# Kernel optimization log

Hardware: AMD Instinct MI355X
Metric: run time of the kernel (lower is better)

The kernel has to match this reference:

```python
import jax, jax.numpy as jnp
import numpy as np

EXPERT_CAPACITY = 1024  # per-batch per-expert capacity (token_priority <= capacity)


def setup_inputs() -> dict:
    key = jax.random.key(0)
    ks = jax.random.split(key, 5)
    B, S, D, FF, E = 2, 4096, 1024, 4096, 8
    return {
        "hidden_states": jax.random.normal(ks[0], (B, S, D), dtype=jnp.float32),
        "gate_w": jax.random.normal(ks[1], (D, E), dtype=jnp.float32) * (1.0 / np.sqrt(D)),
        "w1": jax.random.normal(ks[2], (E, D, FF), dtype=jnp.float32) * (1.0 / np.sqrt(D)),
        "w2": jax.random.normal(ks[3], (E, FF, D), dtype=jnp.float32) * (1.0 / np.sqrt(FF)),
        "w3": jax.random.normal(ks[4], (E, D, FF), dtype=jnp.float32) * (1.0 / np.sqrt(D)),
    }


def reference(hidden_states, gate_w, w1, w2, w3):
    B, S, D = hidden_states.shape
    E = gate_w.shape[1]
    C = EXPERT_CAPACITY

    # ---- route (jitter_noise = 0) ----
    router_logits = jnp.einsum("bsd,de->bse", hidden_states, gate_w)  # [B,S,E]
    router_probs = jax.nn.softmax(router_logits, axis=-1)
    sel = jnp.argmax(router_probs, axis=-1)  # [B,S] top-1 expert
    onehot = jax.nn.one_hot(sel, E, dtype=jnp.int32)  # [B,S,E]
    priority = jnp.cumsum(onehot, axis=1)  # cumsum over sequence (dim=-2)
    # position of token in its chosen expert's buffer (0-based)
    pos = jnp.take_along_axis(priority, sel[..., None], axis=-1)[..., 0] - 1  # [B,S]
    keep = pos < C  # token_priority <= expert_capacity
    max_prob = jnp.max(router_probs, axis=-1, keepdims=True)  # [B,S,1]

    # ---- dispatch: scatter kept tokens into [B,E,C,D]; dropped tokens have pos>=C -> mode='drop'
    b_idx = jnp.broadcast_to(jnp.arange(B)[:, None], (B, S))
    buf = jnp.zeros((B, E, C, D), dtype=hidden_states.dtype)
    buf = buf.at[b_idx, sel, pos].set(hidden_states, mode="drop")

    # ---- per-expert gated MLP (grouped GEMM): act(x@w1) * (x@w3) @ w2 ----
    g = jax.nn.silu(jnp.einsum("becd,edf->becf", buf, w1))
    u = jnp.einsum("becd,edf->becf", buf, w3)
    expert_out = jnp.einsum("becf,efd->becd", g * u, w2)  # [B,E,C,D]

    # ---- combine: kept tokens get expert output, dropped tokens keep hidden_states ----
    pos_g = jnp.minimum(pos, C - 1)  # safe gather index for dropped tokens
    gathered = expert_out[b_idx, sel, pos_g]  # [B,S,D]
    next_states = jnp.where(keep[..., None], gathered, hidden_states)
    out = max_prob * next_states  # dropout is identity (p=0)
    return out, router_logits
```

## Files before the change

kernel.cpp:

```cpp
#include <hip/hip_runtime.h>
#include <hip/hip_bf16.h>
#include <stdint.h>

#define B_  2
#define S_  4096
#define D_  1024
#define FF_ 4096
#define E_  8
#define C_  1024

typedef unsigned short u16;
typedef unsigned int   u32;
typedef float f32x4  __attribute__((ext_vector_type(4)));
typedef short bf16x8 __attribute__((ext_vector_type(8)));
typedef u16   u16x8  __attribute__((ext_vector_type(8)));

static __device__ __forceinline__ u16 f2bf(float f) {
    union { float f; u32 u; } v; v.f = f;
    u32 u = v.u;
    u32 r = (u + 0x7FFFu + ((u >> 16) & 1u)) >> 16;
    return (u16)r;
}

static __device__ __forceinline__ void gload_lds16(const u16* g, u16* l) {
    __builtin_amdgcn_global_load_lds(
        (const __attribute__((address_space(1))) u32*)g,
        (__attribute__((address_space(3))) u32*)l, 16, 0, 0);
}

#define BAR()    asm volatile("s_barrier" ::: "memory")
#define WAITV(n) asm volatile("s_waitcnt vmcnt(" #n ")" ::: "memory")

__global__ __launch_bounds__(256) void transpose_cvt(const float* __restrict__ src,
                                                     u16* __restrict__ dst, int K, int N) {
    __shared__ u16 t[64 * 64];
    size_t mat = (size_t)blockIdx.z * K * N;
    int n0 = blockIdx.x * 64, k0 = blockIdx.y * 64;
    int l = threadIdx.x & 63, w = threadIdx.x >> 6;
#pragma unroll
    for (int p = 0; p < 2; ++p) {
        int k = p * 32 + w * 8 + ((l >> 4) << 1);
        int n = (l & 15) * 4;
        float4 v0 = *(const float4*)&src[mat + (size_t)(k0 + k) * N + n0 + n];
        float4 v1 = *(const float4*)&src[mat + (size_t)(k0 + k + 1) * N + n0 + n];
        float a0[4] = {v0.x, v0.y, v0.z, v0.w};
        float a1[4] = {v1.x, v1.y, v1.z, v1.w};
#pragma unroll
        for (int j = 0; j < 4; ++j) {
            int nn = n + j;
            u32 pk = (u32)f2bf(a0[j]) | ((u32)f2bf(a1[j]) << 16);
            int slot = (k >> 3) ^ ((nn & 7) ^ ((nn >> 3) & 7));
            *(u32*)((char*)t + nn * 128 + slot * 16 + (k & 7) * 2) = pk;
        }
    }
    __syncthreads();
#pragma unroll
    for (int p = 0; p < 2; ++p) {
        int n = p * 32 + (threadIdx.x >> 3);
        int k8 = threadIdx.x & 7;
        int slot = k8 ^ ((n & 7) ^ ((n >> 3) & 7));
        u16x8 v = *(u16x8*)((char*)t + n * 128 + slot * 16);
        *(u16x8*)&dst[mat + (size_t)(n0 + n) * K + k0 + k8 * 8] = v;
    }
}

__global__ __launch_bounds__(256) void router_kernel(const float* __restrict__ hidden,
                                                     const float* __restrict__ gate_w,
                                                     float* __restrict__ logits_out,
                                                     int* __restrict__ sel,
                                                     float* __restrict__ maxp,
                                                     u16* __restrict__ xbf) {
    __shared__ float gw[D_ * E_];
    for (int i = threadIdx.x; i < D_ * E_ / 4; i += 256)
        ((float4*)gw)[i] = ((const float4*)gate_w)[i];
    __syncthreads();

    int wave = threadIdx.x >> 6, lane = threadIdx.x & 63;
    int tok = blockIdx.x * 4 + wave;
    const float* hrow = hidden + (size_t)tok * D_;
    u16* xrow = xbf + (size_t)tok * D_;

    double acc[8] = {0, 0, 0, 0, 0, 0, 0, 0};
#pragma unroll 4
    for (int i = 0; i < D_ / 64; i++) {
        int d = i * 64 + lane;
        float h = hrow[d];
        xrow[d] = f2bf(h);
        const float4* g4 = (const float4*)(gw + d * 8);
        float4 g0 = g4[0], g1 = g4[1];
        acc[0] += (double)h * g0.x; acc[1] += (double)h * g0.y;
        acc[2] += (double)h * g0.z; acc[3] += (double)h * g0.w;
        acc[4] += (double)h * g1.x; acc[5] += (double)h * g1.y;
        acc[6] += (double)h * g1.z; acc[7] += (double)h * g1.w;
    }
#pragma unroll
    for (int off = 32; off > 0; off >>= 1)
#pragma unroll
        for (int e = 0; e < 8; e++)
            acc[e] += __shfl_xor(acc[e], off);

    float l[8];
#pragma unroll
    for (int e = 0; e < 8; e++) l[e] = (float)acc[e];
    if (lane < 8) logits_out[(size_t)tok * 8 + lane] = l[lane];

    int am = 0; float mx = l[0];
#pragma unroll
    for (int e = 1; e < 8; e++) if (l[e] > mx) { mx = l[e]; am = e; }
    float sum = 0.f;
#pragma unroll
    for (int e = 0; e < 8; e++) sum += expf(l[e] - mx);
    if (lane == 0) { sel[tok] = am; maxp[tok] = 1.0f / sum; }
}

__global__ void scan_kernel(const int* __restrict__ sel, int* __restrict__ pos,
                            int* __restrict__ slot_token, int* __restrict__ counts) {
    int wave = threadIdx.x >> 6, lane = threadIdx.x & 63;
    int b = wave;
    int carry[8] = {0, 0, 0, 0, 0, 0, 0, 0};
    unsigned long long below = (lane == 0) ? 0ull : ((~0ull) >> (64 - lane));
    for (int s0 = 0; s0 < S_; s0 += 64) {
        int s = s0 + lane;
        int e = sel[b * S_ + s];
        int p = 0;
#pragma unroll
        for (int ex = 0; ex < 8; ex++) {
            unsigned long long m = __ballot(e == ex);
            if (e == ex) p = carry[ex] + (int)__popcll(m & below);
            carry[ex] += (int)__popcll(m);
        }
        pos[b * S_ + s] = p;
        if (p < C_) slot_token[(b * E_ + e) * C_ + p] = s;
    }
    if (lane < 8) {
        int c = carry[lane];
        counts[b * E_ + lane] = c < C_ ? c : C_;
    }
}

__global__ __launch_bounds__(512, 2) void gemm1_kernel(const u16* __restrict__ x,
                                                       const u16* __restrict__ w1t,
                                                       const u16* __restrict__ w3t,
                                                       const int* __restrict__ slot_token,
                                                       const int* __restrict__ counts,
                                                       u16* __restrict__ hbuf) {
    extern __shared__ u16 lds[];
    int phys = blockIdx.x + 32 * (blockIdx.y + 4 * blockIdx.z);
    int virt = (phys & 7) * 256 + (phys >> 3);
    int bx = virt & 31, by = (virt >> 5) & 3, bz = virt >> 7;

    int z = bz;
    int cnt = counts[z];
    int c0 = by * 256;
    if (c0 >= cnt) return;
    int n0 = bx * 128;
    int b = z >> 3, e = z & 7;

    int tid = threadIdx.x, w = tid >> 6, l = tid & 63;
    int wm = w >> 2, wn = w & 3;

    int arow0 = tid >> 2, arow1 = arow0 + 128;
    int lk = ((tid & 3) ^ ((tid >> 3) & 3)) * 8;
    int as0 = c0 + arow0, as1 = c0 + arow1;
    int tok0 = slot_token[z * C_ + (as0 < cnt ? as0 : 0)];
    int tok1 = slot_token[z * C_ + (as1 < cnt ? as1 : 0)];
    const u16* pA0 = x + ((size_t)(b * S_ + tok0)) * D_ + lk;
    const u16* pA1 = x + ((size_t)(b * S_ + tok1)) * D_ + lk;
    const u16* pB1 = w1t + ((size_t)e * FF_ + n0 + arow0) * D_ + lk;
    const u16* pB3 = w3t + ((size_t)e * FF_ + n0 + arow0) * D_ + lk;
    u32 wsl = (u32)w * 512;

    u32 ck  = (u32)(((l >> 4) ^ ((l >> 1) & 3)) * 8);
    u32 aoff  = (u32)(wm * 128 + (l & 15)) * 32 + ck;
    u32 b1off = 8192  + (u32)(wn * 32 + (l & 15)) * 32 + ck;
    u32 b3off = 12288 + (u32)(wn * 32 + (l & 15)) * 32 + ck;

    auto STAGE = [&](int t) {
        u16* Ls = lds + ((t & 3) << 14);
        int ko = t << 5;
        gload_lds16(pA0 + ko, Ls + wsl);
        gload_lds16(pA1 + ko, Ls + 4096 + wsl);
        gload_lds16(pB1 + ko, Ls + 8192 + wsl);
        gload_lds16(pB3 + ko, Ls + 12288 + wsl);
    };

    f32x4 acc1[8][2] = {};
    f32x4 acc3[8][2] = {};

    constexpr int NK = D_ / 32;
    STAGE(0); STAGE(1); STAGE(2);
    for (int t = 0; t < NK; ++t) {
        if (t + 2 < NK)      { WAITV(8); }
        else if (t + 1 < NK) { WAITV(4); }
        else                 { WAITV(0); }
        BAR();
        if (t + 3 < NK) STAGE(t + 3);
        const u16* Ls = lds + ((t & 3) << 14);
        bf16x8 af[8], b1f[2], b3f[2];
#pragma unroll
        for (int f = 0; f < 8; f++) af[f] = *(const bf16x8*)(Ls + aoff + f * 512);
#pragma unroll
        for (int n = 0; n < 2; n++) {
            b1f[n] = *(const bf16x8*)(Ls + b1off + n * 512);
            b3f[n] = *(const bf16x8*)(Ls + b3off + n * 512);
        }
        __builtin_amdgcn_s_setprio(1);
#pragma unroll
        for (int f = 0; f < 8; f++)
#pragma unroll
            for (int n = 0; n < 2; n++) {
                acc1[f][n] = __builtin_amdgcn_mfma_f32_16x16x32_bf16(af[f], b1f[n], acc1[f][n], 0, 0, 0);
                acc3[f][n] = __builtin_amdgcn_mfma_f32_16x16x32_bf16(af[f], b3f[n], acc3[f][n], 0, 0, 0);
            }
        __builtin_amdgcn_s_setprio(0);
    }

#pragma unroll
    for (int f = 0; f < 8; f++) {
        int row = wm * 128 + f * 16 + ((l >> 4) << 2);
#pragma unroll
        for (int r = 0; r < 4; r++) {
            int slot = c0 + row + r;
            if (slot < cnt) {
                size_t base = ((size_t)z * C_ + slot) * FF_ + n0 + wn * 32 + (l & 15);
#pragma unroll
                for (int n = 0; n < 2; n++) {
                    float g = acc1[f][n][r], uu = acc3[f][n][r];
                    float h = (g / (1.f + __expf(-g))) * uu;
                    hbuf[base + n * 16] = f2bf(h);
                }
            }
        }
    }
}

__global__ __launch_bounds__(512, 2) void gemm2_kernel(const u16* __restrict__ hbuf,
                                                       const u16* __restrict__ w2t,
                                                       const int* __restrict__ slot_token,
                                                       const int* __restrict__ counts,
                                                       const float* __restrict__ maxp,
                                                       float* __restrict__ out) {
    extern __shared__ u16 lds[];
    int phys = blockIdx.x + 4 * (blockIdx.y + 4 * blockIdx.z);
    int virt = (phys & 7) * 32 + (phys >> 3);
    int bx = virt & 3, by = (virt >> 2) & 3, bz = virt >> 4;

    int z = bz;
    int cnt = counts[z];
    int c0 = by * 256;
    if (c0 >= cnt) return;
    int n0 = bx * 256;
    int b = z >> 3, e = z & 7;

    int tid = threadIdx.x, w = tid >> 6, l = tid & 63;
    int wm = w >> 2, wn = w & 3;

    int arow0 = tid >> 2;
    int lk = ((tid & 3) ^ ((tid >> 3) & 3)) * 8;
    const u16* pA0 = hbuf + ((size_t)z * C_ + c0 + arow0) * FF_ + lk;
    const u16* pA1 = pA0 + (size_t)128 * FF_;
    const u16* pB0 = w2t + ((size_t)e * D_ + n0 + arow0) * FF_ + lk;
    const u16* pB1 = pB0 + (size_t)128 * FF_;
    u32 wsl = (u32)w * 512;

    u32 ck  = (u32)(((l >> 4) ^ ((l >> 1) & 3)) * 8);
    u32 aoff = (u32)(wm * 128 + (l & 15)) * 32 + ck;
    u32 boff = 8192 + (u32)(wn * 64 + (l & 15)) * 32 + ck;

    auto STAGE = [&](int t) {
        u16* Ls = lds + ((t & 3) << 14);
        int ko = t << 5;
        gload_lds16(pA0 + ko, Ls + wsl);
        gload_lds16(pA1 + ko, Ls + 4096 + wsl);
        gload_lds16(pB0 + ko, Ls + 8192 + wsl);
        gload_lds16(pB1 + ko, Ls + 12288 + wsl);
    };

    f32x4 acc[8][4] = {};

    constexpr int NK = FF_ / 32;
    STAGE(0); STAGE(1); STAGE(2);
    for (int t = 0; t < NK; ++t) {
        if (t + 2 < NK)      { WAITV(8); }
        else if (t + 1 < NK) { WAITV(4); }
        else                 { WAITV(0); }
        BAR();
        if (t + 3 < NK) STAGE(t + 3);
        const u16* Ls = lds + ((t & 3) << 14);
        bf16x8 af[8], bfv[4];
#pragma unroll
        for (int f = 0; f < 8; f++) af[f] = *(const bf16x8*)(Ls + aoff + f * 512);
#pragma unroll
        for (int n = 0; n < 4; n++) bfv[n] = *(const bf16x8*)(Ls + boff + n * 512);
        __builtin_amdgcn_s_setprio(1);
#pragma unroll
        for (int f = 0; f < 8; f++)
#pragma unroll
            for (int n = 0; n < 4; n++)
                acc[f][n] = __builtin_amdgcn_mfma_f32_16x16x32_bf16(af[f], bfv[n], acc[f][n], 0, 0, 0);
        __builtin_amdgcn_s_setprio(0);
    }

#pragma unroll
    for (int f = 0; f < 8; f++) {
        int row = wm * 128 + f * 16 + ((l >> 4) << 2);
#pragma unroll
        for (int r = 0; r < 4; r++) {
            int slot = c0 + row + r;
            if (slot < cnt) {
                int s = slot_token[z * C_ + slot];
                float sc = maxp[b * S_ + s];
                float* orow = out + ((size_t)b * S_ + s) * D_ + n0 + wn * 64 + (l & 15);
#pragma unroll
                for (int n = 0; n < 4; n++)
                    orow[n * 16] = sc * acc[f][n][r];
            }
        }
    }
}

__global__ __launch_bounds__(256) void combine_dropped(const float* __restrict__ hidden,
                                                       const int* __restrict__ pos,
                                                       const float* __restrict__ maxp,
                                                       float* __restrict__ out) {
    int t = blockIdx.x;
    if (pos[t] < C_) return;
    float sc = maxp[t];
    const float* src = hidden + (size_t)t * D_;
    float* dst = out + (size_t)t * D_;
    for (int d = threadIdx.x; d < D_; d += 256) dst[d] = sc * src[d];
}

extern "C" void kernel_launch(void* const* d_in, const int* in_sizes, int n_in,
                              void* d_out, int out_size, void* d_ws, size_t ws_size,
                              hipStream_t stream) {
    const float* hidden = (const float*)d_in[0];
    const float* gate_w = (const float*)d_in[1];
    const float* w1     = (const float*)d_in[2];
    const float* w2     = (const float*)d_in[3];
    const float* w3     = (const float*)d_in[4];

    float* out        = (float*)d_out;
    float* logits_out = out + (size_t)B_ * S_ * D_;

    char* ws = (char*)d_ws;
    u16* hidden_bf = (u16*)ws;            ws += (size_t)B_ * S_ * D_ * 2;
    u16* w1t       = (u16*)ws;            ws += (size_t)E_ * D_ * FF_ * 2;
    u16* w3t       = (u16*)ws;            ws += (size_t)E_ * D_ * FF_ * 2;
    u16* w2t       = (u16*)ws;            ws += (size_t)E_ * D_ * FF_ * 2;
    u16* hbuf      = (u16*)ws;            ws += (size_t)B_ * E_ * C_ * FF_ * 2;
    int*   sel        = (int*)ws;         ws += (size_t)B_ * S_ * 4;
    int*   pos        = (int*)ws;         ws += (size_t)B_ * S_ * 4;
    float* maxp       = (float*)ws;       ws += (size_t)B_ * S_ * 4;
    int*   slot_token = (int*)ws;         ws += (size_t)B_ * E_ * C_ * 4;
    int*   counts     = (int*)ws;         ws += (size_t)B_ * E_ * 4;

    (void)hipFuncSetAttribute((const void*)gemm1_kernel,
                              hipFuncAttributeMaxDynamicSharedMemorySize, 131072);
    (void)hipFuncSetAttribute((const void*)gemm2_kernel,
                              hipFuncAttributeMaxDynamicSharedMemorySize, 131072);

    router_kernel<<<B_ * S_ / 4, 256, 0, stream>>>(hidden, gate_w, logits_out, sel, maxp, hidden_bf);
    scan_kernel<<<1, 128, 0, stream>>>(sel, pos, slot_token, counts);

    transpose_cvt<<<dim3(FF_ / 64, D_ / 64, E_), 256, 0, stream>>>(w1, w1t, D_, FF_);
    transpose_cvt<<<dim3(FF_ / 64, D_ / 64, E_), 256, 0, stream>>>(w3, w3t, D_, FF_);
    transpose_cvt<<<dim3(D_ / 64, FF_ / 64, E_), 256, 0, stream>>>(w2, w2t, FF_, D_);

    gemm1_kernel<<<dim3(32, 4, 16), 512, 131072, stream>>>(hidden_bf, w1t, w3t, slot_token, counts, hbuf);
    gemm2_kernel<<<dim3(4, 4, 16), 512, 131072, stream>>>(hbuf, w2t, slot_token, counts, maxp, out);
    combine_dropped<<<B_ * S_, 256, 0, stream>>>(hidden, pos, maxp, out);
}
```

Before: 501.2 us.

## Split GEMM k-step into two phases interleaving stage loads with MFMA halves

Each k-iteration of both expert GEMMs is split into two halves. The first half loads half the A fragments and all B fragments, issues the A-tile prefetch for stage t+3, waits on LDS and runs half the MFMAs. A second barrier follows, then the remaining A fragments are read, the B-tile prefetch is issued and the rest of the MFMAs run. The aim is to interleave global-to-LDS traffic with matrix math and spread out LDS reads, at the cost of an extra barrier and explicit lgkmcnt waits per iteration.

```diff
diff --git a/kernel.cpp b/kernel.cpp
--- a/kernel.cpp
+++ b/kernel.cpp
@@ -30,6 +30,8 @@
 
 #define BAR()    asm volatile("s_barrier" ::: "memory")
 #define WAITV(n) asm volatile("s_waitcnt vmcnt(" #n ")" ::: "memory")
+#define WAITL0() do { asm volatile("s_waitcnt lgkmcnt(0)" ::: "memory"); \
+                      __builtin_amdgcn_sched_barrier(0); } while (0)
 
 __global__ __launch_bounds__(256) void transpose_cvt(const float* __restrict__ src,
                                                      u16* __restrict__ dst, int K, int N) {
@@ -175,11 +177,15 @@
     u32 b1off = 8192  + (u32)(wn * 32 + (l & 15)) * 32 + ck;
     u32 b3off = 12288 + (u32)(wn * 32 + (l & 15)) * 32 + ck;
 
-    auto STAGE = [&](int t) {
+    auto STAGE_A = [&](int t) {
         u16* Ls = lds + ((t & 3) << 14);
         int ko = t << 5;
         gload_lds16(pA0 + ko, Ls + wsl);
         gload_lds16(pA1 + ko, Ls + 4096 + wsl);
+    };
+    auto STAGE_B = [&](int t) {
+        u16* Ls = lds + ((t & 3) << 14);
+        int ko = t << 5;
         gload_lds16(pB1 + ko, Ls + 8192 + wsl);
         gload_lds16(pB3 + ko, Ls + 12288 + wsl);
     };
@@ -188,25 +194,40 @@
     f32x4 acc3[8][2] = {};
 
     constexpr int NK = D_ / 32;
-    STAGE(0); STAGE(1); STAGE(2);
+    STAGE_A(0); STAGE_B(0); STAGE_A(1); STAGE_B(1); STAGE_A(2); STAGE_B(2);
     for (int t = 0; t < NK; ++t) {
         if (t + 2 < NK)      { WAITV(8); }
         else if (t + 1 < NK) { WAITV(4); }
         else                 { WAITV(0); }
         BAR();
-        if (t + 3 < NK) STAGE(t + 3);
         const u16* Ls = lds + ((t & 3) << 14);
         bf16x8 af[8], b1f[2], b3f[2];
 #pragma unroll
-        for (int f = 0; f < 8; f++) af[f] = *(const bf16x8*)(Ls + aoff + f * 512);
+        for (int f = 0; f < 4; f++) af[f] = *(const bf16x8*)(Ls + aoff + f * 512);
 #pragma unroll
         for (int n = 0; n < 2; n++) {
             b1f[n] = *(const bf16x8*)(Ls + b1off + n * 512);
             b3f[n] = *(const bf16x8*)(Ls + b3off + n * 512);
         }
+        if (t + 3 < NK) STAGE_A(t + 3);
+        WAITL0();
         __builtin_amdgcn_s_setprio(1);
 #pragma unroll
-        for (int f = 0; f < 8; f++)
+        for (int f = 0; f < 4; f++)
+#pragma unroll
+            for (int n = 0; n < 2; n++) {
+                acc1[f][n] = __builtin_amdgcn_mfma_f32_16x16x32_bf16(af[f], b1f[n], acc1[f][n], 0, 0, 0);
+                acc3[f][n] = __builtin_amdgcn_mfma_f32_16x16x32_bf16(af[f], b3f[n], acc3[f][n], 0, 0, 0);
+            }
+        __builtin_amdgcn_s_setprio(0);
+        BAR();
+#pragma unroll
+        for (int f = 4; f < 8; f++) af[f] = *(const bf16x8*)(Ls + aoff + f * 512);
+        if (t + 3 < NK) STAGE_B(t + 3);
+        WAITL0();
+        __builtin_amdgcn_s_setprio(1);
+#pragma unroll
+        for (int f = 4; f < 8; f++)
 #pragma unroll
             for (int n = 0; n < 2; n++) {
                 acc1[f][n] = __builtin_amdgcn_mfma_f32_16x16x32_bf16(af[f], b1f[n], acc1[f][n], 0, 0, 0);
@@ -267,11 +288,15 @@
     u32 aoff = (u32)(wm * 128 + (l & 15)) * 32 + ck;
     u32 boff = 8192 + (u32)(wn * 64 + (l & 15)) * 32 + ck;
 
-    auto STAGE = [&](int t) {
+    auto STAGE_A = [&](int t) {
         u16* Ls = lds + ((t & 3) << 14);
         int ko = t << 5;
         gload_lds16(pA0 + ko, Ls + wsl);
         gload_lds16(pA1 + ko, Ls + 4096 + wsl);
+    };
+    auto STAGE_B = [&](int t) {
+        u16* Ls = lds + ((t & 3) << 14);
+        int ko = t << 5;
         gload_lds16(pB0 + ko, Ls + 8192 + wsl);
         gload_lds16(pB1 + ko, Ls + 12288 + wsl);
     };
@@ -279,22 +304,35 @@
     f32x4 acc[8][4] = {};
 
     constexpr int NK = FF_ / 32;
-    STAGE(0); STAGE(1); STAGE(2);
+    STAGE_A(0); STAGE_B(0); STAGE_A(1); STAGE_B(1); STAGE_A(2); STAGE_B(2);
     for (int t = 0; t < NK; ++t) {
         if (t + 2 < NK)      { WAITV(8); }
         else if (t + 1 < NK) { WAITV(4); }
         else                 { WAITV(0); }
         BAR();
-        if (t + 3 < NK) STAGE(t + 3);
         const u16* Ls = lds + ((t & 3) << 14);
         bf16x8 af[8], bfv[4];
 #pragma unroll
-        for (int f = 0; f < 8; f++) af[f] = *(const bf16x8*)(Ls + aoff + f * 512);
+        for (int f = 0; f < 4; f++) af[f] = *(const bf16x8*)(Ls + aoff + f * 512);
 #pragma unroll
         for (int n = 0; n < 4; n++) bfv[n] = *(const bf16x8*)(Ls + boff + n * 512);
+        if (t + 3 < NK) STAGE_A(t + 3);
+        WAITL0();
         __builtin_amdgcn_s_setprio(1);
 #pragma unroll
-        for (int f = 0; f < 8; f++)
+        for (int f = 0; f < 4; f++)
+#pragma unroll
+            for (int n = 0; n < 4; n++)
+                acc[f][n] = __builtin_amdgcn_mfma_f32_16x16x32_bf16(af[f], bfv[n], acc[f][n], 0, 0, 0);
+        __builtin_amdgcn_s_setprio(0);
+        BAR();
+#pragma unroll
+        for (int f = 4; f < 8; f++) af[f] = *(const bf16x8*)(Ls + aoff + f * 512);
+        if (t + 3 < NK) STAGE_B(t + 3);
+        WAITL0();
+        __builtin_amdgcn_s_setprio(1);
+#pragma unroll
+        for (int f = 4; f < 8; f++)
 #pragma unroll
             for (int n = 0; n < 4; n++)
                 acc[f][n] = __builtin_amdgcn_mfma_f32_16x16x32_bf16(af[f], bfv[n], acc[f][n], 0, 0, 0);
```

After: 490.8 us. -2.1%, faster.
